# Kernel optimization log

Measured on AMD Instinct MI355X. Metric: run time of the kernel, lower is better.

The kernel has to match this reference:

```python
import jax, jax.numpy as jnp
import numpy as np

N, E, B, F, H = 100000, 800000, 128, 128, 128
G = 5
INV_BN = np.float32(1.0 / np.sqrt(1.0 + 1e-5))  # eval BatchNorm, running_mean=0, running_var=1

_HEAD_SHAPES = [("norm_emb_g", (2*H,)), ("norm_emb_b", (2*H,)),
                ("fc1_W", (16, 2*H+1)), ("fc1_b", (16,)),
                ("bn1_g", (16,)), ("bn1_b", (16,)),
                ("fc2_W", (2, 2*H+3)), ("fc2_b", (2,)),
                ("fc3a_W", (4, 2*H+5)), ("fc3a_b", (4,)),
                ("fc3b_W", (5, 2*H+5)), ("fc3b_b", (5,)),
                ("normc_g", (2*H+5,)), ("normc_b", (2*H+5,))]


def setup_inputs() -> dict:
    key = jax.random.key(0)
    ks = jax.random.split(key, 64)
    p = lambda i, shape: jax.random.normal(ks[i], shape, jnp.float32) * 0.05
    inp = {
        "x": jax.random.normal(ks[0], (N, F), jnp.float32),
        "edge_index": jax.random.randint(ks[1], (2, E), 0, N, dtype=jnp.int32),
        "edge_direction": jax.random.randint(ks[2], (E,), 0, 2, dtype=jnp.int32),
        "batch": jnp.sort(jax.random.randint(ks[3], (N,), 0, B, dtype=jnp.int32)),
        "graph_feature": jax.random.normal(ks[4], (B, G), jnp.float32),
        "task": 1,
    }
    i = 5
    for pref in ("pre", "suc"):
        for l in range(3):
            inp[pref + "_Wl%d" % l] = p(i, (H, H)); i += 1
            inp[pref + "_bl%d" % l] = p(i, (H,)); i += 1
            inp[pref + "_Wr%d" % l] = p(i, (H, H)); i += 1
    for name, shape in _HEAD_SHAPES:
        inp[name] = p(i, shape); i += 1
    return inp


def reference(x, edge_index, edge_direction, batch, graph_feature, task,
              pre_Wl0, pre_bl0, pre_Wr0, pre_Wl1, pre_bl1, pre_Wr1, pre_Wl2, pre_bl2, pre_Wr2,
              suc_Wl0, suc_bl0, suc_Wr0, suc_Wl1, suc_bl1, suc_Wr1, suc_Wl2, suc_bl2, suc_Wr2,
              norm_emb_g, norm_emb_b, fc1_W, fc1_b, bn1_g, bn1_b, fc2_W, fc2_b,
              fc3a_W, fc3a_b, fc3b_W, fc3b_b, normc_g, normc_b):
    src, dst = edge_index[0], edge_index[1]
    pre_mask = (edge_direction == 0).astype(x.dtype)
    suc_mask = (edge_direction == 1).astype(x.dtype)

    def sage(h, mask, Wl, bl, Wr):
        # PyG SAGEConv: lin_l(scatter_mean(x[src] -> dst)) + lin_r(h); masked edges emulate
        # the edge_direction slicing without data-dependent shapes.
        msg = h[src] * mask[:, None]                              # [E, H]
        agg = jax.ops.segment_sum(msg, dst, num_segments=N)      # [N, H]
        cnt = jax.ops.segment_sum(mask, dst, num_segments=N)     # [N]
        mean = agg / jnp.maximum(cnt, 1.0)[:, None]
        return mean @ Wl.T + bl + h @ Wr.T

    bn = lambda v, g, b: g * (v * INV_BN) + b  # eval-mode BatchNorm1d after reset

    pre_x, suc_x = x, x
    for Wl, bl, Wr in ((pre_Wl0, pre_bl0, pre_Wr0), (pre_Wl1, pre_bl1, pre_Wr1), (pre_Wl2, pre_bl2, pre_Wr2)):
        pre_x = jax.nn.relu(sage(pre_x, pre_mask, Wl, bl, Wr))
    for Wl, bl, Wr in ((suc_Wl0, suc_bl0, suc_Wr0), (suc_Wl1, suc_bl1, suc_Wr1), (suc_Wl2, suc_bl2, suc_Wr2)):
        suc_x = jax.nn.relu(sage(suc_x, suc_mask, Wl, bl, Wr))

    comb = jnp.concatenate([pre_x, suc_x], axis=1)               # [N, 2H]
    gsum = jax.ops.segment_sum(comb, batch, num_segments=B)
    gcnt = jax.ops.segment_sum(jnp.ones((N,), comb.dtype), batch, num_segments=B)
    combined = bn(gsum / jnp.maximum(gcnt, 1.0)[:, None], norm_emb_g, norm_emb_b)  # [B, 2H]

    lev_lsb = graph_feature[:, -1:]
    nx3 = graph_feature[:, -3:]
    out1 = bn(jax.nn.relu(jnp.concatenate([combined, lev_lsb], 1) @ fc1_W.T + fc1_b), bn1_g, bn1_b)
    out2 = jax.nn.relu(jnp.concatenate([combined, nx3], 1) @ fc2_W.T + fc2_b)
    pred = jnp.argmax(out2, axis=1)

    wf1 = graph_feature[:, 2:3]
    wf2 = graph_feature[:, 1:2]
    x3 = bn(jnp.concatenate([combined, wf1, wf2, nx3], 1), normc_g, normc_b)
    b1 = x3 @ fc3a_W.T + fc3a_b                                  # [B, 4]
    b2 = x3 @ fc3b_W.T + fc3b_b                                  # [B, 5]
    out3 = jnp.concatenate([jnp.where((pred == 0)[:, None], b1, 0.0),
                            jnp.where((pred == 1)[:, None], b2, 0.0)], axis=1)  # [B, 9]
    return (out1, out2, out3)
```

## Files before the change

kernel.cpp:

```cpp
#include <hip/hip_runtime.h>

constexpr int kN = 100000;
constexpr int kNpad = 100096;
constexpr int kE = 800000;
constexpr int kB = 128;
constexpr int kBinsPerDir = 391;
constexpr int kNB = 782;
constexpr int kRep = 16;
constexpr int kCtrs = kNB * kRep;
constexpr float kInvBN = 0.99999500003749968f;

constexpr int kXconvBlocks = kNpad * 128 / 4 / 256;
constexpr int kWprepBlocks = 768;
constexpr int kBincountBlocks = (kE + 255) / 256;
constexpr int kGstartBlocks = (kN + 255) / 256;
constexpr int kPrepBlocks = kXconvBlocks + kWprepBlocks + kBincountBlocks + kGstartBlocks;

typedef short s16x8 __attribute__((ext_vector_type(8)));
typedef float f32x4 __attribute__((ext_vector_type(4)));

__device__ inline ushort bf16rne(float f) {
  uint u = __builtin_bit_cast(uint, f);
  u += 0x7fffu + ((u >> 16) & 1u);
  return (ushort)(u >> 16);
}
__device__ inline float bflo(uint v) { return __builtin_bit_cast(float, v << 16); }
__device__ inline float bfhi(uint v) { return __builtin_bit_cast(float, v & 0xffff0000u); }
__device__ inline uint pack2(float a, float b) {
  return (uint)bf16rne(a) | ((uint)bf16rne(b) << 16);
}

struct WPtrs { const float* Wl[6]; const float* Wr[6]; };


__global__ __launch_bounds__(256) void prep_kernel(
    const float* __restrict__ x, ushort* __restrict__ xb,
    WPtrs p, ushort* __restrict__ Wb,
    const int* __restrict__ ei, const int* __restrict__ ed,
    int* __restrict__ bincnt,
    const int* __restrict__ batch, int* __restrict__ gstart) {
  int bi = blockIdx.x;
  int t = threadIdx.x;
  if (bi < kXconvBlocks) {
    int i4 = (bi * 256 + t) * 4;
    ushort4 r;
    if (i4 < kN * 128) {
      float4 v = *(const float4*)&x[i4];
      r.x = bf16rne(v.x); r.y = bf16rne(v.y); r.z = bf16rne(v.z); r.w = bf16rne(v.w);
    } else {
      r.x = r.y = r.z = r.w = 0;
    }
    *(ushort4*)&xb[i4] = r;
  } else if (bi < kXconvBlocks + kWprepBlocks) {
    int id = (bi - kXconvBlocks) * 256 + t;
    int L = id >> 15;
    int o = (id >> 8) & 127, k = id & 255;
    const float* src = (k < 128) ? p.Wl[L] : p.Wr[L];
    Wb[id] = bf16rne(src[o * 128 + (k & 127)]);
  } else if (bi < kXconvBlocks + kWprepBlocks + kBincountBlocks) {
    int e = (bi - kXconvBlocks - kWprepBlocks) * 256 + t;
    if (e < kE) {
      int dst = ei[kE + e];
      int ctr = (ed[e] * kBinsPerDir + (dst >> 8)) * kRep + ((e >> 8) & 15);
      atomicAdd(&bincnt[ctr], 1);
    }
  } else {
    int n = (bi - kXconvBlocks - kWprepBlocks - kBincountBlocks) * 256 + t;
    if (n < kN) {
      int b = batch[n];
      int bprev = (n == 0) ? -1 : batch[n - 1];
      for (int g = bprev + 1; g <= b; ++g) gstart[g] = n;
      if (n == kN - 1)
        for (int g = b + 1; g <= kB; ++g) gstart[g] = kN;
    }
  }
}


__global__ __launch_bounds__(256) void scan1_kernel(const int* __restrict__ in,
                                                    int* __restrict__ out,
                                                    int* __restrict__ bsum, int M) {
  __shared__ int s[256];
  int t = threadIdx.x;
  int idx = blockIdx.x * 1024 + t * 4;
  int4 v = {0, 0, 0, 0};
  if (idx < M) v = *(const int4*)&in[idx];
  int tsum = v.x + v.y + v.z + v.w;
  s[t] = tsum;
  __syncthreads();
  for (int d = 1; d < 256; d <<= 1) {
    int tmp = (t >= d) ? s[t - d] : 0;
    __syncthreads();
    s[t] += tmp;
    __syncthreads();
  }
  int excl = s[t] - tsum;
  if (idx < M) {
    int4 o;
    o.x = excl; o.y = excl + v.x; o.z = o.y + v.y; o.w = o.z + v.z;
    *(int4*)&out[idx] = o;
  }
  if (t == 255) bsum[blockIdx.x] = s[255];
}

__global__ __launch_bounds__(256) void scan2_kernel(int* __restrict__ bsum, int nb) {
  __shared__ int s[256];
  int t = threadIdx.x;
  int v = (t < nb) ? bsum[t] : 0;
  s[t] = v;
  __syncthreads();
  for (int d = 1; d < 256; d <<= 1) {
    int tmp = (t >= d) ? s[t - d] : 0;
    __syncthreads();
    s[t] += tmp;
    __syncthreads();
  }
  if (t < nb) bsum[t] = s[t] - v;
}

__global__ __launch_bounds__(256) void scan3_kernel(int* __restrict__ out,
                                                    const int* __restrict__ bsum, int M) {
  int idx = blockIdx.x * 1024 + threadIdx.x * 4;
  int add = bsum[blockIdx.x];
  if (idx < M) {
    int4 o = *(int4*)&out[idx];
    o.x += add; o.y += add; o.z += add; o.w += add;
    *(int4*)&out[idx] = o;
  }
}


__global__ __launch_bounds__(256) void binscatter_kernel(const int* __restrict__ ei,
                                                         const int* __restrict__ ed,
                                                         const int* __restrict__ binoff,
                                                         int* __restrict__ bincur,
                                                         uint* __restrict__ binbuf) {
  int e = blockIdx.x * 256 + threadIdx.x;
  if (e >= kE) return;
  int dst = ei[kE + e];
  int ctr = (ed[e] * kBinsPerDir + (dst >> 8)) * kRep + ((e >> 8) & 15);
  int pos = atomicAdd(&bincur[ctr], 1);
  binbuf[binoff[ctr] + pos] = (uint)ei[e] | ((uint)(dst & 255) << 17);
}

__global__ __launch_bounds__(256) void binfill_kernel(const uint* __restrict__ binbuf,
                                                      const int* __restrict__ binoff,
                                                      int* __restrict__ csr,
                                                      int* __restrict__ cnt,
                                                      int* __restrict__ off) {
  __shared__ int lcnt[256];
  __shared__ int ls[256];
  __shared__ int lpos[256];
  int b = blockIdx.x;
  int t = threadIdx.x;
  int dir = (b >= kBinsPerDir) ? 1 : 0;
  int nodeBase = (b - dir * kBinsPerDir) << 8;
  int e0 = binoff[b * kRep];
  int e1 = (b == kNB - 1) ? kE : binoff[(b + 1) * kRep];
  lcnt[t] = 0;
  __syncthreads();
  for (int e = e0 + t; e < e1; e += 256) atomicAdd(&lcnt[binbuf[e] >> 17], 1);
  __syncthreads();
  int my = lcnt[t];
  ls[t] = my;
  __syncthreads();
  for (int d = 1; d < 256; d <<= 1) {
    int tmp = (t >= d) ? ls[t - d] : 0;
    __syncthreads();
    ls[t] += tmp;
    __syncthreads();
  }
  int excl = ls[t] - my;
  lpos[t] = e0 + excl;
  int node = nodeBase + t;
  if (node < kN) {
    int g = dir * kN + node;
    cnt[g] = my;
    off[g] = e0 + excl;
  }
  __syncthreads();
  for (int e = e0 + t; e < e1; e += 256) {
    uint v = binbuf[e];
    int pos = atomicAdd(&lpos[v >> 17], 1);
    csr[pos] = (int)(v & 0x1FFFFu);
  }
}


__global__ __launch_bounds__(512) void fused_layer_kernel(
    const ushort* __restrict__ h,
    ushort* __restrict__ outp,
    const ushort* __restrict__ Wb,
    const float* __restrict__ bl,
    const int* __restrict__ off,
    const int* __restrict__ cnt,
    const int* __restrict__ csr,
    int dirbase) {
  __shared__ ushort Wlds[128 * 256];

  const int t = threadIdx.x;
#pragma unroll
  for (int it = 0; it < 8; ++it) {
    int u = t + 512 * it;
    int o = u >> 5, b = u & 31;
    uint4 v = *(const uint4*)(Wb + (size_t)u * 8);
    *(uint4*)((char*)Wlds + o * 512 + ((b ^ (o & 7)) << 4)) = v;
  }

  const int w = t >> 6;
  const int l = t & 63;
  const int lr = l & 15;
  const int lq = l >> 4;
  const int node = blockIdx.x * 128 + w * 16 + lr;
  const int swz = lr & 7;

  float ga[32];
#pragma unroll
  for (int i = 0; i < 32; ++i) ga[i] = 0.f;
  int c = 0;
  if (node < kN) {
    int bkt = dirbase + node;
    int s = off[bkt];
    c = cnt[bkt];
    const ushort* hp = h + lq * 8;
    int e = 0;
    for (; e + 2 <= c; e += 2) {
      int s0 = csr[s + e];
      int s1 = csr[s + e + 1];
      const ushort* p0 = hp + (size_t)s0 * 128;
      const ushort* p1 = hp + (size_t)s1 * 128;
      uint4 va[4], vb[4];
#pragma unroll
      for (int q = 0; q < 4; ++q) va[q] = *(const uint4*)(p0 + q * 32);
#pragma unroll
      for (int q = 0; q < 4; ++q) vb[q] = *(const uint4*)(p1 + q * 32);
#pragma unroll
      for (int q = 0; q < 4; ++q) {
        ga[q * 8 + 0] += bflo(va[q].x) + bflo(vb[q].x);
        ga[q * 8 + 1] += bfhi(va[q].x) + bfhi(vb[q].x);
        ga[q * 8 + 2] += bflo(va[q].y) + bflo(vb[q].y);
        ga[q * 8 + 3] += bfhi(va[q].y) + bfhi(vb[q].y);
        ga[q * 8 + 4] += bflo(va[q].z) + bflo(vb[q].z);
        ga[q * 8 + 5] += bfhi(va[q].z) + bfhi(vb[q].z);
        ga[q * 8 + 6] += bflo(va[q].w) + bflo(vb[q].w);
        ga[q * 8 + 7] += bfhi(va[q].w) + bfhi(vb[q].w);
      }
    }
    if (e < c) {
      int s0 = csr[s + e];
      const ushort* p0 = hp + (size_t)s0 * 128;
      uint4 va[4];
#pragma unroll
      for (int q = 0; q < 4; ++q) va[q] = *(const uint4*)(p0 + q * 32);
#pragma unroll
      for (int q = 0; q < 4; ++q) {
        ga[q * 8 + 0] += bflo(va[q].x);
        ga[q * 8 + 1] += bfhi(va[q].x);
        ga[q * 8 + 2] += bflo(va[q].y);
        ga[q * 8 + 3] += bfhi(va[q].y);
        ga[q * 8 + 4] += bflo(va[q].z);
        ga[q * 8 + 5] += bfhi(va[q].z);
        ga[q * 8 + 6] += bflo(va[q].w);
        ga[q * 8 + 7] += bfhi(va[q].w);
      }
    }
  }
  float iv = 1.0f / fmaxf((float)c, 1.0f);
  s16x8 am[4];
#pragma unroll
  for (int q = 0; q < 4; ++q) {
    uint4 r;
    r.x = pack2(ga[q * 8 + 0] * iv, ga[q * 8 + 1] * iv);
    r.y = pack2(ga[q * 8 + 2] * iv, ga[q * 8 + 3] * iv);
    r.z = pack2(ga[q * 8 + 4] * iv, ga[q * 8 + 5] * iv);
    r.w = pack2(ga[q * 8 + 6] * iv, ga[q * 8 + 7] * iv);
    am[q] = __builtin_bit_cast(s16x8, r);
  }

  __syncthreads();

  f32x4 acc[8];
#pragma unroll
  for (int j = 0; j < 8; ++j) acc[j] = {0.f, 0.f, 0.f, 0.f};

#pragma unroll
  for (int kk = 0; kk < 8; ++kk) {
    s16x8 a;
    if (kk < 4) {
      a = am[kk];
    } else {
      a = *(const s16x8*)(h + (size_t)node * 128 + (kk - 4) * 32 + lq * 8);
    }
    const int ks = (kk * 4 + lq) ^ swz;
#pragma unroll
    for (int j = 0; j < 8; ++j) {
      int o = j * 16 + lr;
      s16x8 wf = *(const s16x8*)((const char*)Wlds + o * 512 + (ks << 4));
      acc[j] = __builtin_amdgcn_mfma_f32_16x16x32_bf16(wf, a, acc[j], 0, 0, 0);
    }
  }

  if (node < kN) {
#pragma unroll
    for (int j = 0; j < 8; ++j) {
      int o = j * 16 + lq * 4;
      float4 bv = *(const float4*)(bl + o);
      ushort4 r;
      r.x = bf16rne(fmaxf(acc[j][0] + bv.x, 0.f));
      r.y = bf16rne(fmaxf(acc[j][1] + bv.y, 0.f));
      r.z = bf16rne(fmaxf(acc[j][2] + bv.z, 0.f));
      r.w = bf16rne(fmaxf(acc[j][3] + bv.w, 0.f));
      *(ushort4*)(outp + (size_t)node * 128 + o) = r;
    }
  }
}


__global__ __launch_bounds__(256) void pool_kernel(const ushort* __restrict__ h,
                                                   const int* __restrict__ gstart,
                                                   float* __restrict__ comb_raw,
                                                   int base) {
  __shared__ float part[4 * 128];
  int gb = blockIdx.x;
  int graph = gb >> 4;
  int chunk = gb & 15;
  int t = threadIdx.x;
  int slice = t >> 6;
  int col = t & 63;
  int s = gstart[graph];
  int e = gstart[graph + 1];
  int len = e - s;
  int c0 = s + (int)((long long)len * chunk / 16);
  int c1 = s + (int)((long long)len * (chunk + 1) / 16);
  float ax = 0.f, ay = 0.f;
  for (int n = c0 + slice; n < c1; n += 4) {
    uint v = *(const uint*)(h + (size_t)n * 128 + col * 2);
    ax += bflo(v);
    ay += bfhi(v);
  }
  part[slice * 128 + col * 2] = ax;
  part[slice * 128 + col * 2 + 1] = ay;
  __syncthreads();
  if (t < 128) {
    float v = part[t] + part[128 + t] + part[256 + t] + part[384 + t];
    atomicAdd(&comb_raw[graph * 256 + base + t], v);
  }
}


__global__ __launch_bounds__(256) void head_kernel(
    const float* __restrict__ comb_raw, const int* __restrict__ gstart,
    const float* __restrict__ gf,
    const float* __restrict__ neg, const float* __restrict__ neb,
    const float* __restrict__ fc1W, const float* __restrict__ fc1b,
    const float* __restrict__ bn1g, const float* __restrict__ bn1b,
    const float* __restrict__ fc2W, const float* __restrict__ fc2b,
    const float* __restrict__ fc3aW, const float* __restrict__ fc3ab,
    const float* __restrict__ fc3bW, const float* __restrict__ fc3bb,
    const float* __restrict__ ncg, const float* __restrict__ ncb,
    float* __restrict__ out) {
  __shared__ float wlds[6979];
  __shared__ float comb[256];
  __shared__ float x3[261];
  __shared__ float r2s[2];

  const int b = blockIdx.x;
  const int t = threadIdx.x;

  for (int i = t; i < 4112; i += 256) wlds[i] = fc1W[i];
  for (int i = t; i < 518; i += 256) wlds[4112 + i] = fc2W[i];
  for (int i = t; i < 1044; i += 256) wlds[4630 + i] = fc3aW[i];
  for (int i = t; i < 1305; i += 256) wlds[5674 + i] = fc3bW[i];

  float cntf = fmaxf((float)(gstart[b + 1] - gstart[b]), 1.0f);
  if (t < 256) comb[t] = neg[t] * ((comb_raw[b * 256 + t] / cntf) * kInvBN) + neb[t];
  __syncthreads();

  float g1 = gf[b * 5 + 1], g2 = gf[b * 5 + 2], g3 = gf[b * 5 + 3], g4 = gf[b * 5 + 4];
  const int g = t >> 3, l8 = t & 7;

  {
    float p = 0.f;
    if (g < 16) {
      const float* w = &wlds[g * 257];
      for (int j = l8; j < 256; j += 8) p += comb[j] * w[j];
    } else if (g < 18) {
      const float* w = &wlds[4112 + (g - 16) * 259];
      for (int j = l8; j < 256; j += 8) p += comb[j] * w[j];
    }
    p += __shfl_xor(p, 1);
    p += __shfl_xor(p, 2);
    p += __shfl_xor(p, 4);
    if (l8 == 0) {
      if (g < 16) {
        float z = fmaxf(p + wlds[g * 257 + 256] * g4 + fc1b[g], 0.f);
        out[b * 16 + g] = bn1g[g] * (z * kInvBN) + bn1b[g];
      } else if (g < 18) {
        int o = g - 16;
        const float* w = &wlds[4112 + o * 259];
        float z = fmaxf(p + w[256] * g2 + w[257] * g3 + w[258] * g4 + fc2b[o], 0.f);
        out[2048 + b * 2 + o] = z;
        r2s[o] = z;
      }
    }
  }
  for (int j = t; j < 261; j += 256) {
    float v;
    if (j < 256) v = comb[j];
    else if (j == 256) v = g2;
    else if (j == 257) v = g1;
    else if (j == 258) v = g2;
    else if (j == 259) v = g3;
    else v = g4;
    x3[j] = ncg[j] * (v * kInvBN) + ncb[j];
  }
  __syncthreads();
  int pred = (r2s[1] > r2s[0]) ? 1 : 0;

  {
    float p = 0.f;
    if (g < 4) {
      const float* w = &wlds[4630 + g * 261];
      for (int j = l8; j < 261; j += 8) p += x3[j] * w[j];
    } else if (g < 9) {
      const float* w = &wlds[5674 + (g - 4) * 261];
      for (int j = l8; j < 261; j += 8) p += x3[j] * w[j];
    }
    p += __shfl_xor(p, 1);
    p += __shfl_xor(p, 2);
    p += __shfl_xor(p, 4);
    if (l8 == 0) {
      if (g < 4) {
        float v = p + fc3ab[g];
        out[2304 + b * 9 + g] = (pred == 0) ? v : 0.f;
      } else if (g < 9) {
        int o = g - 4;
        float v = p + fc3bb[o];
        out[2304 + b * 9 + 4 + o] = (pred == 1) ? v : 0.f;
      }
    }
  }
}


extern "C" void kernel_launch(void* const* d_in, const int* in_sizes, int n_in,
                              void* d_out, int out_size, void* d_ws, size_t ws_size,
                              hipStream_t stream) {
  (void)in_sizes; (void)n_in; (void)out_size; (void)ws_size;
  const float* x   = (const float*)d_in[0];
  const int* ei    = (const int*)d_in[1];
  const int* ed    = (const int*)d_in[2];
  const int* batch = (const int*)d_in[3];
  const float* gf  = (const float*)d_in[4];

  char* ws = (char*)d_ws;
  auto carve = [&](size_t bytes) -> void* {
    void* p = ws;
    ws += (bytes + 255) & ~(size_t)255;
    return p;
  };
  int* cnt        = (int*)carve(2 * kN * sizeof(int));
  int* off        = (int*)carve(2 * kN * sizeof(int));
  int* bincnt     = (int*)carve(kCtrs * sizeof(int));
  int* bincur     = (int*)carve(kCtrs * sizeof(int));
  int* binoff     = (int*)carve((kCtrs + 4) * sizeof(int));
  int* bsum       = (int*)carve(1024);
  int* gstart     = (int*)carve((kB + 1) * sizeof(int));
  int* csr        = (int*)carve(kE * sizeof(int));
  uint* binbuf    = (uint*)carve(kE * sizeof(uint));
  float* comb_raw = (float*)carve(kB * 256 * sizeof(float));
  ushort* xb      = (ushort*)carve((size_t)kNpad * 128 * 2);
  ushort* buf0    = (ushort*)carve((size_t)kNpad * 128 * 2);
  ushort* buf1    = (ushort*)carve((size_t)kNpad * 128 * 2);
  ushort* Wb      = (ushort*)carve(6 * 128 * 256 * 2);

  hipMemsetAsync(bincnt, 0, kCtrs * sizeof(int), stream);
  hipMemsetAsync(bincur, 0, kCtrs * sizeof(int), stream);
  hipMemsetAsync(comb_raw, 0, kB * 256 * sizeof(float), stream);

  WPtrs wp;
  for (int L = 0; L < 6; ++L) {
    wp.Wl[L] = (const float*)d_in[6 + 3 * L];
    wp.Wr[L] = (const float*)d_in[6 + 3 * L + 2];
  }

  prep_kernel<<<kPrepBlocks, 256, 0, stream>>>(x, xb, wp, Wb, ei, ed, bincnt, batch, gstart);

  constexpr int NBScan = (kCtrs + 1023) / 1024;
  scan1_kernel<<<NBScan, 256, 0, stream>>>(bincnt, binoff, bsum, kCtrs);
  scan2_kernel<<<1, 256, 0, stream>>>(bsum, NBScan);
  scan3_kernel<<<NBScan, 256, 0, stream>>>(binoff, bsum, kCtrs);
  binscatter_kernel<<<(kE + 255) / 256, 256, 0, stream>>>(ei, ed, binoff, bincur, binbuf);
  binfill_kernel<<<kNB, 256, 0, stream>>>(binbuf, binoff, csr, cnt, off);

  auto layerF = [&](const ushort* hin, ushort* hout, int L, int dirbase) {
    fused_layer_kernel<<<kNpad / 128, 512, 0, stream>>>(
        hin, hout, Wb + (size_t)L * 32768, (const float*)d_in[6 + 3 * L + 1],
        off, cnt, csr, dirbase);
  };

  layerF(xb,   buf0, 0, 0);
  layerF(buf0, buf1, 1, 0);
  layerF(buf1, buf0, 2, 0);
  pool_kernel<<<kB * 16, 256, 0, stream>>>(buf0, gstart, comb_raw, 0);

  layerF(xb,   buf1, 3, kN);
  layerF(buf1, buf0, 4, kN);
  layerF(buf0, buf1, 5, kN);
  pool_kernel<<<kB * 16, 256, 0, stream>>>(buf1, gstart, comb_raw, 128);

  head_kernel<<<kB, 256, 0, stream>>>(
      comb_raw, gstart, gf,
      (const float*)d_in[24], (const float*)d_in[25],
      (const float*)d_in[26], (const float*)d_in[27],
      (const float*)d_in[28], (const float*)d_in[29],
      (const float*)d_in[30], (const float*)d_in[31],
      (const float*)d_in[32], (const float*)d_in[33],
      (const float*)d_in[34], (const float*)d_in[35],
      (const float*)d_in[36], (const float*)d_in[37],
      (float*)d_out);
}
```

Before: 382.9 us.

## Sort nodes by in-degree so aggregation wavefronts get balanced edge counts

Adds a counting-sort pass (histogram, scan, scatter) that builds a per-direction node permutation ordered by in-degree, capped at 63. The fused layer kernel maps its rows through this permutation, so the 16 nodes sharing a wavefront have similar neighbour counts and the gather loop does not sit idle waiting on the longest list. It also prefetches the self-feature rows before aggregation, and widens the binning replication factor from 16 to 64 to spread atomic contention. The cost is three extra small kernels and less contiguous self-row reads and output writes, since node order is now permuted.

```diff
diff --git a/kernel.cpp b/kernel.cpp
--- a/kernel.cpp
+++ b/kernel.cpp
@@ -6,7 +6,7 @@
 constexpr int kB = 128;
 constexpr int kBinsPerDir = 391;
 constexpr int kNB = 782;
-constexpr int kRep = 16;
+constexpr int kRep = 64;
 constexpr int kCtrs = kNB * kRep;
 constexpr float kInvBN = 0.99999500003749968f;
 
@@ -61,7 +61,7 @@
     int e = (bi - kXconvBlocks - kWprepBlocks) * 256 + t;
     if (e < kE) {
       int dst = ei[kE + e];
-      int ctr = (ed[e] * kBinsPerDir + (dst >> 8)) * kRep + ((e >> 8) & 15);
+      int ctr = ((ed[e] * kBinsPerDir + (dst >> 8)) << 6) | ((e >> 8) & 63);
       atomicAdd(&bincnt[ctr], 1);
     }
   } else {
@@ -138,7 +138,7 @@
   int e = blockIdx.x * 256 + threadIdx.x;
   if (e >= kE) return;
   int dst = ei[kE + e];
-  int ctr = (ed[e] * kBinsPerDir + (dst >> 8)) * kRep + ((e >> 8) & 15);
+  int ctr = ((ed[e] * kBinsPerDir + (dst >> 8)) << 6) | ((e >> 8) & 63);
   int pos = atomicAdd(&bincur[ctr], 1);
   binbuf[binoff[ctr] + pos] = (uint)ei[e] | ((uint)(dst & 255) << 17);
 }
@@ -187,6 +187,67 @@
 }
 
 
+__global__ __launch_bounds__(256) void dhist_kernel(const int* __restrict__ cnt,
+                                                    int* __restrict__ ghist,
+                                                    int* __restrict__ blockbase) {
+  __shared__ int h[64];
+  int b = blockIdx.x;
+  int t = threadIdx.x;
+  int dir = (b >= kBinsPerDir) ? 1 : 0;
+  int node = (b - dir * kBinsPerDir) * 256 + t;
+  if (t < 64) h[t] = 0;
+  __syncthreads();
+  if (node < kN) {
+    int d = cnt[dir * kN + node];
+    atomicAdd(&h[min(d, 63)], 1);
+  }
+  __syncthreads();
+  if (t < 64) blockbase[b * 64 + t] = atomicAdd(&ghist[dir * 64 + t], h[t]);
+}
+
+__global__ __launch_bounds__(64) void dscan_kernel(int* __restrict__ ghist,
+                                                   uint* __restrict__ perm) {
+  __shared__ int s[64];
+  int t = threadIdx.x;
+  for (int dir = 0; dir < 2; ++dir) {
+    int v = ghist[dir * 64 + t];
+    s[t] = v;
+    __syncthreads();
+    for (int d = 1; d < 64; d <<= 1) {
+      int tmp = (t >= d) ? s[t - d] : 0;
+      __syncthreads();
+      s[t] += tmp;
+      __syncthreads();
+    }
+    ghist[dir * 64 + t] = s[t] - v;
+    __syncthreads();
+  }
+  for (int i = t; i < kNpad - kN; i += 64) {
+    perm[kN + i] = kN;
+    perm[kNpad + kN + i] = kN;
+  }
+}
+
+__global__ __launch_bounds__(256) void dscatter_kernel(const int* __restrict__ cnt,
+                                                       const int* __restrict__ ghist,
+                                                       const int* __restrict__ blockbase,
+                                                       uint* __restrict__ perm) {
+  __shared__ int h[64];
+  int b = blockIdx.x;
+  int t = threadIdx.x;
+  int dir = (b >= kBinsPerDir) ? 1 : 0;
+  int node = (b - dir * kBinsPerDir) * 256 + t;
+  if (t < 64) h[t] = 0;
+  __syncthreads();
+  if (node < kN) {
+    int bucket = min(cnt[dir * kN + node], 63);
+    int r = atomicAdd(&h[bucket], 1);
+    int pos = ghist[dir * 64 + bucket] + blockbase[b * 64 + bucket] + r;
+    perm[dir * kNpad + pos] = (uint)node;
+  }
+}
+
+
 __global__ __launch_bounds__(512) void fused_layer_kernel(
     const ushort* __restrict__ h,
     ushort* __restrict__ outp,
@@ -195,6 +256,7 @@
     const int* __restrict__ off,
     const int* __restrict__ cnt,
     const int* __restrict__ csr,
+    const uint* __restrict__ perm,
     int dirbase) {
   __shared__ ushort Wlds[128 * 256];
 
@@ -211,8 +273,13 @@
   const int l = t & 63;
   const int lr = l & 15;
   const int lq = l >> 4;
-  const int node = blockIdx.x * 128 + w * 16 + lr;
+  const int node = (int)perm[blockIdx.x * 128 + w * 16 + lr];
   const int swz = lr & 7;
+
+  s16x8 self[4];
+#pragma unroll
+  for (int q = 0; q < 4; ++q)
+    self[q] = *(const s16x8*)(h + (size_t)node * 128 + q * 32 + lq * 8);
 
   float ga[32];
 #pragma unroll
@@ -285,12 +352,7 @@
 
 #pragma unroll
   for (int kk = 0; kk < 8; ++kk) {
-    s16x8 a;
-    if (kk < 4) {
-      a = am[kk];
-    } else {
-      a = *(const s16x8*)(h + (size_t)node * 128 + (kk - 4) * 32 + lq * 8);
-    }
+    s16x8 a = (kk < 4) ? am[kk] : self[kk - 4];
     const int ks = (kk * 4 + lq) ^ swz;
 #pragma unroll
     for (int j = 0; j < 8; ++j) {
@@ -466,6 +528,9 @@
   int* binoff     = (int*)carve((kCtrs + 4) * sizeof(int));
   int* bsum       = (int*)carve(1024);
   int* gstart     = (int*)carve((kB + 1) * sizeof(int));
+  int* ghist      = (int*)carve(128 * sizeof(int));
+  int* blockbase  = (int*)carve(kNB * 64 * sizeof(int));
+  uint* perm      = (uint*)carve(2 * kNpad * sizeof(uint));
   int* csr        = (int*)carve(kE * sizeof(int));
   uint* binbuf    = (uint*)carve(kE * sizeof(uint));
   float* comb_raw = (float*)carve(kB * 256 * sizeof(float));
@@ -476,6 +541,7 @@
 
   hipMemsetAsync(bincnt, 0, kCtrs * sizeof(int), stream);
   hipMemsetAsync(bincur, 0, kCtrs * sizeof(int), stream);
+  hipMemsetAsync(ghist, 0, 128 * sizeof(int), stream);
   hipMemsetAsync(comb_raw, 0, kB * 256 * sizeof(float), stream);
 
   WPtrs wp;
@@ -493,10 +559,14 @@
   binscatter_kernel<<<(kE + 255) / 256, 256, 0, stream>>>(ei, ed, binoff, bincur, binbuf);
   binfill_kernel<<<kNB, 256, 0, stream>>>(binbuf, binoff, csr, cnt, off);
 
-  auto layerF = [&](const ushort* hin, ushort* hout, int L, int dirbase) {
+  dhist_kernel<<<kNB, 256, 0, stream>>>(cnt, ghist, blockbase);
+  dscan_kernel<<<1, 64, 0, stream>>>(ghist, perm);
+  dscatter_kernel<<<kNB, 256, 0, stream>>>(cnt, ghist, blockbase, perm);
+
+  auto layerF = [&](const ushort* hin, ushort* hout, int L, int dir) {
     fused_layer_kernel<<<kNpad / 128, 512, 0, stream>>>(
         hin, hout, Wb + (size_t)L * 32768, (const float*)d_in[6 + 3 * L + 1],
-        off, cnt, csr, dirbase);
+        off, cnt, csr, perm + (size_t)dir * kNpad, dir * kN);
   };
 
   layerF(xb,   buf0, 0, 0);
@@ -504,9 +574,9 @@
   layerF(buf1, buf0, 2, 0);
   pool_kernel<<<kB * 16, 256, 0, stream>>>(buf0, gstart, comb_raw, 0);
 
-  layerF(xb,   buf1, 3, kN);
-  layerF(buf1, buf0, 4, kN);
-  layerF(buf0, buf1, 5, kN);
+  layerF(xb,   buf1, 3, 1);
+  layerF(buf1, buf0, 4, 1);
+  layerF(buf0, buf1, 5, 1);
   pool_kernel<<<kB * 16, 256, 0, stream>>>(buf1, gstart, comb_raw, 128);
 
   head_kernel<<<kB, 256, 0, stream>>>(
```

Result: slower. 419.3 us (+9.5%).
